# Kernel optimization log

Hardware: AMD Instinct MI355X
Metric: run time of the kernel (lower is better)

## Reference

```python
import jax, jax.numpy as jnp
import numpy as np

B, L, D = 2, 2048, 2048
H, KVH, HD = 16, 4, 128
GROUPS = H // KVH  # 4 == KVH (required by this module's v_proj sizing)
EPS = 1e-6
SCALE = HD ** -0.5
NEG = -1e9


def setup_inputs() -> dict:
    key = jax.random.key(0)
    ks = jax.random.split(key, 6)
    hidden_states = jax.random.normal(ks[0], (B, L, D), jnp.float32)
    # RoPE tables (b, l, head_dim), HF-style: angles duplicated across halves
    half = HD // 2
    inv_freq = 1.0 / (1e6 ** (jnp.arange(half, dtype=jnp.float32) / half))
    ang = jnp.arange(L, dtype=jnp.float32)[:, None] * inv_freq[None, :]  # (L, half)
    emb = jnp.concatenate([ang, ang], axis=-1)  # (L, HD)
    cos = jnp.broadcast_to(jnp.cos(emb)[None], (B, L, HD))
    sin = jnp.broadcast_to(jnp.sin(emb)[None], (B, L, HD))
    # additive causal mask (b,1,l,l)
    m = jnp.triu(jnp.full((L, L), NEG, jnp.float32), k=1)
    attention_mask = jnp.broadcast_to(m[None, None], (B, 1, L, L))
    s = 0.02
    wq = jax.random.normal(ks[1], (H * HD, D), jnp.float32) * s
    wk = jax.random.normal(ks[2], (KVH * HD, D), jnp.float32) * s
    wv = jax.random.normal(ks[3], (KVH * HD, D), jnp.float32) * s
    wo = jax.random.normal(ks[4], (D, H * HD), jnp.float32) * s
    q_norm_w = jnp.ones((HD,), jnp.float32)
    k_norm_w = jnp.ones((HD,), jnp.float32)
    return dict(hidden_states=hidden_states, cos=cos, sin=sin,
                attention_mask=attention_mask, wq=wq, wk=wk, wv=wv, wo=wo,
                q_norm_w=q_norm_w, k_norm_w=k_norm_w)


def _rmsnorm(x, w):
    var = jnp.mean(x * x, axis=-1, keepdims=True)
    return w * (x * jax.lax.rsqrt(var + EPS))


def _rotate_half(x):
    u, v = jnp.split(x, 2, axis=-1)
    return jnp.concatenate([-v, u], axis=-1)


def reference(hidden_states, cos, sin, attention_mask, wq, wk, wv, wo, q_norm_w, k_norm_w):
    b, l, _ = hidden_states.shape
    q = (hidden_states @ wq.T).reshape(b, l, H, HD).transpose(0, 2, 1, 3)   # (b,H,l,hd)
    k = (hidden_states @ wk.T).reshape(b, l, KVH, HD).transpose(0, 2, 1, 3)
    v = (hidden_states @ wv.T).reshape(b, l, KVH, HD).transpose(0, 2, 1, 3)
    q = _rmsnorm(q, q_norm_w)
    k = _rmsnorm(k, k_norm_w)
    c = cos[:, None]  # (b,1,l,hd)
    s = sin[:, None]
    q = q * c + _rotate_half(q) * s
    k = k * c + _rotate_half(k) * s
    # GQA: repeat each kv head GROUPS times consecutively (matches repeat_n)
    k = jnp.repeat(k, GROUPS, axis=1)
    v = jnp.repeat(v, GROUPS, axis=1)
    attn = jnp.einsum('bhqd,bhkd->bhqk', q, k) * SCALE + attention_mask
    attn = jax.nn.softmax(attn, axis=-1)
    out = jnp.einsum('bhqk,bhkd->bhqd', attn, v)
    out = out.transpose(0, 2, 1, 3).reshape(b, l, H * HD)
    return out @ wo.T
```

## Files before the change

kernel.cpp:

```cpp
#include <hip/hip_runtime.h>


#define SEQL 2048
#define DMODEL 2048
#define NH 16
#define NKVH 4
#define HDIM 128
#define SCALE_QK 0.08838834764831845f
#define LOG2E 1.4426950408889634f
#define INFF 3.0e38f

typedef __attribute__((ext_vector_type(8))) short bf16x8;
typedef __attribute__((ext_vector_type(4))) float f32x4;
typedef __attribute__((ext_vector_type(4))) unsigned int u32x4;

__device__ __forceinline__ unsigned short f2bf(float x) {
  union { float f; unsigned u; } v; v.f = x;
  unsigned r = v.u + 0x7fffu + ((v.u >> 16) & 1u);
  return (unsigned short)(r >> 16);
}
__device__ __forceinline__ float bf2f(unsigned short u) {
  union { unsigned u; float f; } v; v.u = ((unsigned)u) << 16;
  return v.f;
}

__global__ __launch_bounds__(256) void cast_kernel(const float* __restrict__ src,
                                                   unsigned short* __restrict__ dst,
                                                   int n8) {
  int i = blockIdx.x * 256 + threadIdx.x;
  if (i >= n8) return;
  const f32x4* s4 = (const f32x4*)src;
  f32x4 a = s4[2 * i], b = s4[2 * i + 1];
  union { unsigned short s[8]; u32x4 v; } o;
  o.s[0] = f2bf(a[0]); o.s[1] = f2bf(a[1]); o.s[2] = f2bf(a[2]); o.s[3] = f2bf(a[3]);
  o.s[4] = f2bf(b[0]); o.s[5] = f2bf(b[1]); o.s[6] = f2bf(b[2]); o.s[7] = f2bf(b[3]);
  ((u32x4*)dst)[i] = o.v;
}

__global__ __launch_bounds__(256) void cast3_kernel(const float* __restrict__ s0,
                                                    const float* __restrict__ s1,
                                                    const float* __restrict__ s2,
                                                    unsigned short* __restrict__ dst,
                                                    int n0, int n1, int n2) {
  int i = blockIdx.x * 256 + threadIdx.x;
  const float* src;
  int j;
  if (i < n0) { src = s0; j = i; }
  else if (i < n0 + n1) { src = s1; j = i - n0; }
  else if (i < n0 + n1 + n2) { src = s2; j = i - n0 - n1; }
  else return;
  const f32x4* s4 = (const f32x4*)src;
  f32x4 a = s4[2 * j], b = s4[2 * j + 1];
  union { unsigned short s[8]; u32x4 v; } o;
  o.s[0] = f2bf(a[0]); o.s[1] = f2bf(a[1]); o.s[2] = f2bf(a[2]); o.s[3] = f2bf(a[3]);
  o.s[4] = f2bf(b[0]); o.s[5] = f2bf(b[1]); o.s[6] = f2bf(b[2]); o.s[7] = f2bf(b[3]);
  ((u32x4*)dst)[i] = o.v;
}

template <int OUT_BF16>
__global__ __launch_bounds__(256) void gemm_bt(const unsigned short* __restrict__ A,
                                               const unsigned short* __restrict__ B,
                                               void* __restrict__ C,
                                               int M, int N, int K) {
  __shared__ unsigned short As[128 * 64];
  __shared__ unsigned short Bs[128 * 64];
  int tid = threadIdx.x;
  int w = tid >> 6, lane = tid & 63;
  int lr = lane & 15, lg = lane >> 4;
  int m0 = blockIdx.y * 128, n0 = blockIdx.x * 128;
  int wr = (w >> 1) * 64, wc = (w & 1) * 64;
  f32x4 zero4 = {0.f, 0.f, 0.f, 0.f};
  f32x4 acc[4][4];
  for (int i = 0; i < 4; ++i)
    for (int j = 0; j < 4; ++j) acc[i][j] = zero4;

  for (int k0 = 0; k0 < K; k0 += 64) {
    __syncthreads();
    for (int i = 0; i < 4; ++i) {
      int o = i * 4096 + w * 1024 + lane * 16;
      int row = o >> 7, cb = o & 127;
      int scb = cb ^ ((row & 7) << 4);
      const char* ga = (const char*)(A + (size_t)(m0 + row) * K + k0) + scb;
      const char* gb = (const char*)(B + (size_t)(n0 + row) * K + k0) + scb;
      __builtin_amdgcn_global_load_lds(
          (const __attribute__((address_space(1))) void*)ga,
          (__attribute__((address_space(3))) void*)((char*)As + i * 4096 + w * 1024),
          16, 0, 0);
      __builtin_amdgcn_global_load_lds(
          (const __attribute__((address_space(1))) void*)gb,
          (__attribute__((address_space(3))) void*)((char*)Bs + i * 4096 + w * 1024),
          16, 0, 0);
    }
    asm volatile("s_waitcnt vmcnt(0)" ::: "memory");
    __syncthreads();

    for (int kk = 0; kk < 2; ++kk) {
      bf16x8 a[4], b[4];
      for (int i = 0; i < 4; ++i) {
        int row = wr + i * 16 + lr;
        int col = kk * 64 + lg * 16;
        a[i] = *(const bf16x8*)((const char*)As + row * 128 + (col ^ ((row & 7) << 4)));
      }
      for (int j = 0; j < 4; ++j) {
        int row = wc + j * 16 + lr;
        int col = kk * 64 + lg * 16;
        b[j] = *(const bf16x8*)((const char*)Bs + row * 128 + (col ^ ((row & 7) << 4)));
      }
      for (int i = 0; i < 4; ++i)
        for (int j = 0; j < 4; ++j)
          acc[i][j] = __builtin_amdgcn_mfma_f32_16x16x32_bf16(a[i], b[j], acc[i][j], 0, 0, 0);
    }
  }

  for (int i = 0; i < 4; ++i)
    for (int j = 0; j < 4; ++j) {
      int row = m0 + wr + i * 16 + lg * 4;
      int col = n0 + wc + j * 16 + lr;
      for (int r = 0; r < 4; ++r) {
        if (OUT_BF16)
          ((unsigned short*)C)[(size_t)(row + r) * N + col] = f2bf(acc[i][j][r]);
        else
          ((float*)C)[(size_t)(row + r) * N + col] = acc[i][j][r];
      }
    }
}

__global__ __launch_bounds__(64) void prep_kernel(const unsigned short* __restrict__ qkv,
                                                  const float* __restrict__ cosb,
                                                  const float* __restrict__ sinb,
                                                  const float* __restrict__ qw,
                                                  const float* __restrict__ kw,
                                                  unsigned short* __restrict__ Qb,
                                                  unsigned short* __restrict__ Kb,
                                                  unsigned short* __restrict__ Vtb)
{
  int l = blockIdx.x, b = blockIdx.y, d = threadIdx.x;
  size_t row = (size_t)b * SEQL + l;
  const unsigned short* src = qkv + row * 3072;
  float c0 = cosb[row * HDIM + d], c1 = cosb[row * HDIM + d + 64];
  float s0 = sinb[row * HDIM + d], s1 = sinb[row * HDIM + d + 64];
  float qw0 = qw[d], qw1 = qw[d + 64];
  float kw0 = kw[d], kw1 = kw[d + 64];
  const float qscale = SCALE_QK * LOG2E;

  for (int h = 0; h < NH; ++h) {
    float x0 = bf2f(src[h * HDIM + d]), x1 = bf2f(src[h * HDIM + d + 64]);
    float ss = x0 * x0 + x1 * x1;
    for (int m = 1; m < 64; m <<= 1) ss += __shfl_xor(ss, m);
    float inv = rsqrtf(ss * (1.0f / 128.0f) + 1e-6f);
    float n0 = x0 * inv * qw0, n1 = x1 * inv * qw1;
    float r0 = (n0 * c0 - n1 * s0) * qscale;
    float r1 = (n1 * c1 + n0 * s1) * qscale;
    unsigned short* dst = Qb + (((size_t)(b * NH + h)) * SEQL + l) * HDIM;
    dst[d] = f2bf(r0);
    dst[d + 64] = f2bf(r1);
  }
  for (int h = 0; h < NKVH; ++h) {
    float x0 = bf2f(src[2048 + h * HDIM + d]), x1 = bf2f(src[2048 + h * HDIM + d + 64]);
    float ss = x0 * x0 + x1 * x1;
    for (int m = 1; m < 64; m <<= 1) ss += __shfl_xor(ss, m);
    float inv = rsqrtf(ss * (1.0f / 128.0f) + 1e-6f);
    float n0 = x0 * inv * kw0, n1 = x1 * inv * kw1;
    float r0 = n0 * c0 - n1 * s0;
    float r1 = n1 * c1 + n0 * s1;
    unsigned short* dst = Kb + (((size_t)(b * NKVH + h)) * SEQL + l) * HDIM;
    dst[d] = f2bf(r0);
    dst[d + 64] = f2bf(r1);
  }
  for (int h = 0; h < NKVH; ++h) {
    unsigned short v0 = src[2560 + h * HDIM + d];
    unsigned short v1 = src[2560 + h * HDIM + d + 64];
    unsigned short* dst = Vtb + ((size_t)(b * NKVH + h) * HDIM) * SEQL;
    dst[(size_t)d * SEQL + l] = v0;
    dst[(size_t)(d + 64) * SEQL + l] = v1;
  }
}

__global__ __launch_bounds__(512) void flash_kernel(const unsigned short* __restrict__ Qb,
                                                    const unsigned short* __restrict__ Kb,
                                                    const unsigned short* __restrict__ Vtb,
                                                    unsigned short* __restrict__ AOb)
{
  __shared__ unsigned short Ks[2][64 * 128];
  __shared__ unsigned short Vs[2][128 * 64];
  __shared__ unsigned short Ps[128 * 64];

  int tid = threadIdx.x, w = tid >> 6, lane = tid & 63;
  int lr = lane & 15, lg = lane >> 4;
  int bh = blockIdx.y;
  int qt = (bh < 16) ? (int)blockIdx.x : 15 - (int)blockIdx.x;
  int b = bh >> 4, h = bh & 15, hk = h >> 2;
  int q0 = qt * 128;
  int qrow_base = 16 * w + lg * 4;

  const unsigned short* Qg =
      Qb + (((size_t)(b * NH + h)) * SEQL + q0 + 16 * w + lr) * HDIM + lg * 8;
  bf16x8 aq[4];
  for (int kk = 0; kk < 4; ++kk) aq[kk] = *(const bf16x8*)(Qg + kk * 32);

  const unsigned short* Kg0 = Kb + ((size_t)(b * NKVH + hk)) * SEQL * HDIM;
  const unsigned short* Vg0 = Vtb + ((size_t)(b * NKVH + hk)) * HDIM * SEQL;

  float m_run[4], l_part[4];
  f32x4 zero4 = {0.f, 0.f, 0.f, 0.f};
  f32x4 o_acc[8];
  for (int r = 0; r < 4; ++r) { m_run[r] = -INFF; l_part[r] = 0.f; }
  for (int f = 0; f < 8; ++f) o_acc[f] = zero4;

  int nt = 2 * qt + 2;

  u32x4 kr[2], vr[2];

  auto load_tile = [&](int tt) {
    int k0n = tt * 64;
    for (int i = 0; i < 2; ++i) {
      int o = i * 8192 + tid * 16;
      kr[i] = *(const u32x4*)((const char*)Kg0 + (size_t)(k0n + (o >> 8)) * 256 + (o & 255));
      vr[i] = *(const u32x4*)((const char*)Vg0 +
                              (size_t)(o >> 7) * (SEQL * 2) + (size_t)k0n * 2 + (o & 127));
    }
  };
  auto stage_tile = [&](char* kb, char* vb) {
    for (int i = 0; i < 2; ++i) {
      int o = i * 8192 + tid * 16;
      int krow = o >> 8;
      *(u32x4*)(kb + (o ^ ((krow & 7) << 4))) = kr[i];
      int vrow = o >> 7;
      *(u32x4*)(vb + (o ^ ((vrow & 7) << 4))) = vr[i];
    }
  };
  auto compute_tile = [&](int t, const char* kb, const char* vb) {
    int k0 = t * 64;
    if (k0 > q0 + 16 * w + 15) return;
    bool needmask = (k0 + 63 > q0 + 16 * w);

    f32x4 s[4];
    for (int j = 0; j < 4; ++j) s[j] = zero4;
    __builtin_amdgcn_s_setprio(1);
    for (int kk = 0; kk < 4; ++kk)
      for (int j = 0; j < 4; ++j) {
        int row = j * 16 + lr;
        bf16x8 bk = *(const bf16x8*)(kb +
                     ((row * 256 + kk * 64 + lg * 16) ^ ((lr & 7) << 4)));
        s[j] = __builtin_amdgcn_mfma_f32_16x16x32_bf16(aq[kk], bk, s[j], 0, 0, 0);
      }
    __builtin_amdgcn_s_setprio(0);

    for (int r = 0; r < 4; ++r) {
      int qrow = qrow_base + r;
      float v[4];
      if (needmask) {
        int qg = q0 + qrow;
        for (int j = 0; j < 4; ++j)
          v[j] = (k0 + j * 16 + lr <= qg) ? s[j][r] : -INFF;
      } else {
        for (int j = 0; j < 4; ++j) v[j] = s[j][r];
      }
      float mxl = fmaxf(fmaxf(v[0], v[1]), fmaxf(v[2], v[3]));
      if (!__all(mxl <= m_run[r] + 8.f)) {
        float mx = mxl;
        mx = fmaxf(mx, __shfl_xor(mx, 1));
        mx = fmaxf(mx, __shfl_xor(mx, 2));
        mx = fmaxf(mx, __shfl_xor(mx, 4));
        mx = fmaxf(mx, __shfl_xor(mx, 8));
        float m_new = fmaxf(m_run[r], mx);
        float sc = __builtin_amdgcn_exp2f(m_run[r] - m_new);
        l_part[r] *= sc;
        for (int f = 0; f < 8; ++f) o_acc[f][r] *= sc;
        m_run[r] = m_new;
      }
      float m_use = m_run[r];
      float rs = 0.f;
      for (int j = 0; j < 4; ++j) {
        float p = __builtin_amdgcn_exp2f(v[j] - m_use);
        rs += p;
        *(unsigned short*)((char*)Ps +
            ((qrow * 128 + (j * 16 + lr) * 2) ^ ((qrow & 7) << 4))) = f2bf(p);
      }
      l_part[r] += rs;
    }

    __builtin_amdgcn_s_setprio(1);
    for (int kk = 0; kk < 2; ++kk) {
      int prow = 16 * w + lr;
      bf16x8 ap = *(const bf16x8*)((const char*)Ps +
                   ((prow * 128 + kk * 64 + lg * 16) ^ ((lr & 7) << 4)));
      for (int f = 0; f < 8; ++f) {
        int vrow = f * 16 + lr;
        bf16x8 bv = *(const bf16x8*)(vb +
                     ((vrow * 128 + kk * 64 + lg * 16) ^ ((lr & 7) << 4)));
        o_acc[f] = __builtin_amdgcn_mfma_f32_16x16x32_bf16(ap, bv, o_acc[f], 0, 0, 0);
      }
    }
    __builtin_amdgcn_s_setprio(0);
  };

  load_tile(0);
  stage_tile((char*)Ks[0], (char*)Vs[0]);
  if (nt > 1) load_tile(1);
  asm volatile("s_waitcnt lgkmcnt(0)" ::: "memory");
  __builtin_amdgcn_s_barrier();
  __builtin_amdgcn_sched_barrier(0);

  for (int t = 0; t < nt; t += 2) {
    if (t + 1 < nt) stage_tile((char*)Ks[1], (char*)Vs[1]);
    if (t + 2 < nt) load_tile(t + 2);
    compute_tile(t, (const char*)Ks[0], (const char*)Vs[0]);
    asm volatile("s_waitcnt lgkmcnt(0)" ::: "memory");
    __builtin_amdgcn_s_barrier();
    __builtin_amdgcn_sched_barrier(0);
    if (t + 1 >= nt) break;
    if (t + 2 < nt) stage_tile((char*)Ks[0], (char*)Vs[0]);
    if (t + 3 < nt) load_tile(t + 3);
    compute_tile(t + 1, (const char*)Ks[1], (const char*)Vs[1]);
    asm volatile("s_waitcnt lgkmcnt(0)" ::: "memory");
    __builtin_amdgcn_s_barrier();
    __builtin_amdgcn_sched_barrier(0);
  }

  unsigned short* dst = AOb + ((size_t)b * SEQL + q0) * DMODEL + h * HDIM;
  for (int r = 0; r < 4; ++r) {
    float l = l_part[r];
    l += __shfl_xor(l, 1);
    l += __shfl_xor(l, 2);
    l += __shfl_xor(l, 4);
    l += __shfl_xor(l, 8);
    float inv = 1.0f / l;
    for (int f = 0; f < 8; ++f)
      dst[(size_t)(qrow_base + r) * DMODEL + f * 16 + lr] = f2bf(o_acc[f][r] * inv);
  }
}

extern "C" void kernel_launch(void* const* d_in, const int* in_sizes, int n_in,
                              void* d_out, int out_size, void* d_ws, size_t ws_size,
                              hipStream_t stream) {
  const float* hidden = (const float*)d_in[0];
  const float* cosb = (const float*)d_in[1];
  const float* sinb = (const float*)d_in[2];
  const float* wq = (const float*)d_in[4];
  const float* wk = (const float*)d_in[5];
  const float* wv = (const float*)d_in[6];
  const float* wo = (const float*)d_in[7];
  const float* qw = (const float*)d_in[8];
  const float* kw = (const float*)d_in[9];
  float* out = (float*)d_out;

  char* ws = (char*)d_ws;
  unsigned short* Xb    = (unsigned short*)(ws + 0);
  unsigned short* Wqkvb = (unsigned short*)(ws + 16777216);
  unsigned short* QKVb  = (unsigned short*)(ws + 29360128);
  unsigned short* Qbuf  = (unsigned short*)(ws + 54525952);
  unsigned short* Kbuf  = (unsigned short*)(ws + 71303168);
  unsigned short* Vtb   = (unsigned short*)(ws + 75497472);
  unsigned short* AOb   = Xb;
  unsigned short* Wob   = QKVb;

  cast_kernel<<<(8388608 / 8 + 255) / 256, 256, 0, stream>>>(hidden, Xb, 8388608 / 8);
  cast3_kernel<<<(786432 + 255) / 256, 256, 0, stream>>>(wq, wk, wv, Wqkvb,
                                                         524288, 131072, 131072);

  gemm_bt<1><<<dim3(3072 / 128, 4096 / 128), 256, 0, stream>>>(Xb, Wqkvb, QKVb, 4096, 3072, 2048);

  prep_kernel<<<dim3(SEQL, 2), 64, 0, stream>>>(QKVb, cosb, sinb, qw, kw, Qbuf, Kbuf, Vtb);

  cast_kernel<<<(4194304 / 8 + 255) / 256, 256, 0, stream>>>(wo, Wob, 4194304 / 8);

  flash_kernel<<<dim3(SEQL / 128, 2 * NH), 512, 0, stream>>>(Qbuf, Kbuf, Vtb, AOb);

  gemm_bt<0><<<dim3(2048 / 128, 4096 / 128), 256, 0, stream>>>(AOb, Wob, out, 4096, 2048, 2048);
}
```

Before: 239.0 us.

## Give each flash-attention wave two 16-row Q subtiles, halving block size

The flash kernel now runs 4 waves of 256 threads instead of 8, and each wave handles 32 query rows as two 16-row subtiles, A and B. Each K and V fragment read from LDS then feeds two MFMAs, which halves LDS reads per unit of MFMA work and gives more independent MFMA chains. Cooperative tile loads now issue four 16-byte loads per thread instead of two. The cost is roughly double the accumulator registers per wave, which may lower occupancy, and fewer waves per block to hide latency. Causal skipping also becomes coarser, at 32 rows per wave.

```diff
diff --git a/kernel.cpp b/kernel.cpp
--- a/kernel.cpp
+++ b/kernel.cpp
@@ -176,7 +176,7 @@
   }
 }
 
-__global__ __launch_bounds__(512) void flash_kernel(const unsigned short* __restrict__ Qb,
+__global__ __launch_bounds__(256) void flash_kernel(const unsigned short* __restrict__ Qb,
                                                     const unsigned short* __restrict__ Kb,
                                                     const unsigned short* __restrict__ Vtb,
                                                     unsigned short* __restrict__ AOb)
@@ -191,105 +191,168 @@
   int qt = (bh < 16) ? (int)blockIdx.x : 15 - (int)blockIdx.x;
   int b = bh >> 4, h = bh & 15, hk = h >> 2;
   int q0 = qt * 128;
-  int qrow_base = 16 * w + lg * 4;
-
-  const unsigned short* Qg =
-      Qb + (((size_t)(b * NH + h)) * SEQL + q0 + 16 * w + lr) * HDIM + lg * 8;
-  bf16x8 aq[4];
-  for (int kk = 0; kk < 4; ++kk) aq[kk] = *(const bf16x8*)(Qg + kk * 32);
+  int wrow = 32 * w;
+  int qrb = wrow + lg * 4;
+
+  const unsigned short* QgA =
+      Qb + (((size_t)(b * NH + h)) * SEQL + q0 + wrow + lr) * HDIM + lg * 8;
+  bf16x8 aqA[4], aqB[4];
+#pragma unroll
+  for (int kk = 0; kk < 4; ++kk) {
+    aqA[kk] = *(const bf16x8*)(QgA + kk * 32);
+    aqB[kk] = *(const bf16x8*)(QgA + 16 * HDIM + kk * 32);
+  }
 
   const unsigned short* Kg0 = Kb + ((size_t)(b * NKVH + hk)) * SEQL * HDIM;
   const unsigned short* Vg0 = Vtb + ((size_t)(b * NKVH + hk)) * HDIM * SEQL;
 
-  float m_run[4], l_part[4];
+  float mA[4], lA[4], mB[4], lB[4];
   f32x4 zero4 = {0.f, 0.f, 0.f, 0.f};
-  f32x4 o_acc[8];
-  for (int r = 0; r < 4; ++r) { m_run[r] = -INFF; l_part[r] = 0.f; }
-  for (int f = 0; f < 8; ++f) o_acc[f] = zero4;
+  f32x4 oA[8], oB[8];
+#pragma unroll
+  for (int r = 0; r < 4; ++r) { mA[r] = -INFF; lA[r] = 0.f; mB[r] = -INFF; lB[r] = 0.f; }
+#pragma unroll
+  for (int f = 0; f < 8; ++f) { oA[f] = zero4; oB[f] = zero4; }
 
   int nt = 2 * qt + 2;
 
-  u32x4 kr[2], vr[2];
+  u32x4 kr[4], vr[4];
 
   auto load_tile = [&](int tt) {
     int k0n = tt * 64;
-    for (int i = 0; i < 2; ++i) {
-      int o = i * 8192 + tid * 16;
+#pragma unroll
+    for (int i = 0; i < 4; ++i) {
+      int o = i * 4096 + tid * 16;
       kr[i] = *(const u32x4*)((const char*)Kg0 + (size_t)(k0n + (o >> 8)) * 256 + (o & 255));
       vr[i] = *(const u32x4*)((const char*)Vg0 +
                               (size_t)(o >> 7) * (SEQL * 2) + (size_t)k0n * 2 + (o & 127));
     }
   };
   auto stage_tile = [&](char* kb, char* vb) {
-    for (int i = 0; i < 2; ++i) {
-      int o = i * 8192 + tid * 16;
+#pragma unroll
+    for (int i = 0; i < 4; ++i) {
+      int o = i * 4096 + tid * 16;
       int krow = o >> 8;
       *(u32x4*)(kb + (o ^ ((krow & 7) << 4))) = kr[i];
       int vrow = o >> 7;
       *(u32x4*)(vb + (o ^ ((vrow & 7) << 4))) = vr[i];
     }
   };
+
   auto compute_tile = [&](int t, const char* kb, const char* vb) {
     int k0 = t * 64;
-    if (k0 > q0 + 16 * w + 15) return;
-    bool needmask = (k0 + 63 > q0 + 16 * w);
-
-    f32x4 s[4];
-    for (int j = 0; j < 4; ++j) s[j] = zero4;
+    if (k0 > q0 + wrow + 31) return;
+    bool nmA = (k0 + 63 > q0 + wrow);
+    bool nmB = (k0 + 63 > q0 + wrow + 16);
+
+    f32x4 sA[4], sB[4];
+#pragma unroll
+    for (int j = 0; j < 4; ++j) { sA[j] = zero4; sB[j] = zero4; }
     __builtin_amdgcn_s_setprio(1);
+#pragma unroll
     for (int kk = 0; kk < 4; ++kk)
+#pragma unroll
       for (int j = 0; j < 4; ++j) {
         int row = j * 16 + lr;
         bf16x8 bk = *(const bf16x8*)(kb +
                      ((row * 256 + kk * 64 + lg * 16) ^ ((lr & 7) << 4)));
-        s[j] = __builtin_amdgcn_mfma_f32_16x16x32_bf16(aq[kk], bk, s[j], 0, 0, 0);
+        sA[j] = __builtin_amdgcn_mfma_f32_16x16x32_bf16(aqA[kk], bk, sA[j], 0, 0, 0);
+        sB[j] = __builtin_amdgcn_mfma_f32_16x16x32_bf16(aqB[kk], bk, sB[j], 0, 0, 0);
       }
     __builtin_amdgcn_s_setprio(0);
 
+#pragma unroll
     for (int r = 0; r < 4; ++r) {
-      int qrow = qrow_base + r;
+      int qrow = qrb + r;
       float v[4];
-      if (needmask) {
+      if (nmA) {
         int qg = q0 + qrow;
+#pragma unroll
         for (int j = 0; j < 4; ++j)
-          v[j] = (k0 + j * 16 + lr <= qg) ? s[j][r] : -INFF;
+          v[j] = (k0 + j * 16 + lr <= qg) ? sA[j][r] : -INFF;
       } else {
-        for (int j = 0; j < 4; ++j) v[j] = s[j][r];
+#pragma unroll
+        for (int j = 0; j < 4; ++j) v[j] = sA[j][r];
       }
       float mxl = fmaxf(fmaxf(v[0], v[1]), fmaxf(v[2], v[3]));
-      if (!__all(mxl <= m_run[r] + 8.f)) {
+      if (!__all(mxl <= mA[r] + 8.f)) {
         float mx = mxl;
         mx = fmaxf(mx, __shfl_xor(mx, 1));
         mx = fmaxf(mx, __shfl_xor(mx, 2));
         mx = fmaxf(mx, __shfl_xor(mx, 4));
         mx = fmaxf(mx, __shfl_xor(mx, 8));
-        float m_new = fmaxf(m_run[r], mx);
-        float sc = __builtin_amdgcn_exp2f(m_run[r] - m_new);
-        l_part[r] *= sc;
-        for (int f = 0; f < 8; ++f) o_acc[f][r] *= sc;
-        m_run[r] = m_new;
-      }
-      float m_use = m_run[r];
+        float m_new = fmaxf(mA[r], mx);
+        float sc = __builtin_amdgcn_exp2f(mA[r] - m_new);
+        lA[r] *= sc;
+#pragma unroll
+        for (int f = 0; f < 8; ++f) oA[f][r] *= sc;
+        mA[r] = m_new;
+      }
+      float m_use = mA[r];
       float rs = 0.f;
+#pragma unroll
       for (int j = 0; j < 4; ++j) {
         float p = __builtin_amdgcn_exp2f(v[j] - m_use);
         rs += p;
         *(unsigned short*)((char*)Ps +
             ((qrow * 128 + (j * 16 + lr) * 2) ^ ((qrow & 7) << 4))) = f2bf(p);
       }
-      l_part[r] += rs;
+      lA[r] += rs;
+    }
+#pragma unroll
+    for (int r = 0; r < 4; ++r) {
+      int qrow = qrb + 16 + r;
+      float v[4];
+      if (nmB) {
+        int qg = q0 + qrow;
+#pragma unroll
+        for (int j = 0; j < 4; ++j)
+          v[j] = (k0 + j * 16 + lr <= qg) ? sB[j][r] : -INFF;
+      } else {
+#pragma unroll
+        for (int j = 0; j < 4; ++j) v[j] = sB[j][r];
+      }
+      float mxl = fmaxf(fmaxf(v[0], v[1]), fmaxf(v[2], v[3]));
+      if (!__all(mxl <= mB[r] + 8.f)) {
+        float mx = mxl;
+        mx = fmaxf(mx, __shfl_xor(mx, 1));
+        mx = fmaxf(mx, __shfl_xor(mx, 2));
+        mx = fmaxf(mx, __shfl_xor(mx, 4));
+        mx = fmaxf(mx, __shfl_xor(mx, 8));
+        float m_new = fmaxf(mB[r], mx);
+        float sc = __builtin_amdgcn_exp2f(mB[r] - m_new);
+        lB[r] *= sc;
+#pragma unroll
+        for (int f = 0; f < 8; ++f) oB[f][r] *= sc;
+        mB[r] = m_new;
+      }
+      float m_use = mB[r];
+      float rs = 0.f;
+#pragma unroll
+      for (int j = 0; j < 4; ++j) {
+        float p = __builtin_amdgcn_exp2f(v[j] - m_use);
+        rs += p;
+        *(unsigned short*)((char*)Ps +
+            ((qrow * 128 + (j * 16 + lr) * 2) ^ ((qrow & 7) << 4))) = f2bf(p);
+      }
+      lB[r] += rs;
     }
 
     __builtin_amdgcn_s_setprio(1);
+#pragma unroll
     for (int kk = 0; kk < 2; ++kk) {
-      int prow = 16 * w + lr;
-      bf16x8 ap = *(const bf16x8*)((const char*)Ps +
-                   ((prow * 128 + kk * 64 + lg * 16) ^ ((lr & 7) << 4)));
+      int prA = wrow + lr, prB = wrow + 16 + lr;
+      bf16x8 apA = *(const bf16x8*)((const char*)Ps +
+                    ((prA * 128 + kk * 64 + lg * 16) ^ ((lr & 7) << 4)));
+      bf16x8 apB = *(const bf16x8*)((const char*)Ps +
+                    ((prB * 128 + kk * 64 + lg * 16) ^ ((lr & 7) << 4)));
+#pragma unroll
       for (int f = 0; f < 8; ++f) {
         int vrow = f * 16 + lr;
         bf16x8 bv = *(const bf16x8*)(vb +
                      ((vrow * 128 + kk * 64 + lg * 16) ^ ((lr & 7) << 4)));
-        o_acc[f] = __builtin_amdgcn_mfma_f32_16x16x32_bf16(ap, bv, o_acc[f], 0, 0, 0);
+        oA[f] = __builtin_amdgcn_mfma_f32_16x16x32_bf16(apA, bv, oA[f], 0, 0, 0);
+        oB[f] = __builtin_amdgcn_mfma_f32_16x16x32_bf16(apB, bv, oB[f], 0, 0, 0);
       }
     }
     __builtin_amdgcn_s_setprio(0);
@@ -319,15 +382,29 @@
   }
 
   unsigned short* dst = AOb + ((size_t)b * SEQL + q0) * DMODEL + h * HDIM;
+#pragma unroll
   for (int r = 0; r < 4; ++r) {
-    float l = l_part[r];
+    float l = lA[r];
     l += __shfl_xor(l, 1);
     l += __shfl_xor(l, 2);
     l += __shfl_xor(l, 4);
     l += __shfl_xor(l, 8);
     float inv = 1.0f / l;
+#pragma unroll
     for (int f = 0; f < 8; ++f)
-      dst[(size_t)(qrow_base + r) * DMODEL + f * 16 + lr] = f2bf(o_acc[f][r] * inv);
+      dst[(size_t)(qrb + r) * DMODEL + f * 16 + lr] = f2bf(oA[f][r] * inv);
+  }
+#pragma unroll
+  for (int r = 0; r < 4; ++r) {
+    float l = lB[r];
+    l += __shfl_xor(l, 1);
+    l += __shfl_xor(l, 2);
+    l += __shfl_xor(l, 4);
+    l += __shfl_xor(l, 8);
+    float inv = 1.0f / l;
+#pragma unroll
+    for (int f = 0; f < 8; ++f)
+      dst[(size_t)(qrb + 16 + r) * DMODEL + f * 16 + lr] = f2bf(oB[f][r] * inv);
   }
 }
 
@@ -365,7 +442,7 @@
 
   cast_kernel<<<(4194304 / 8 + 255) / 256, 256, 0, stream>>>(wo, Wob, 4194304 / 8);
 
-  flash_kernel<<<dim3(SEQL / 128, 2 * NH), 512, 0, stream>>>(Qbuf, Kbuf, Vtb, AOb);
+  flash_kernel<<<dim3(SEQL / 128, 2 * NH), 256, 0, stream>>>(Qbuf, Kbuf, Vtb, AOb);
 
   gemm_bt<0><<<dim3(2048 / 128, 4096 / 128), 256, 0, stream>>>(AOb, Wob, out, 4096, 2048, 2048);
 }
```

Result: slower. 302.6 us (+26.6%).
